# Performance work log

Hardware: AMD Instinct MI355X
Metric: run time of the kernel (lower is better)

Reference implementation:

```python
import jax, jax.numpy as jnp
import numpy as np

B, T, C, H = 2, 2048, 1024, 16


def setup_inputs() -> dict:
    key = jax.random.key(0)
    ks = jax.random.split(key, 9)
    s = 1.0 / np.sqrt(C)
    return {
        "query": jax.random.normal(ks[0], (B, T, C), dtype=jnp.float32),
        "Wq": jax.random.normal(ks[1], (C, C), dtype=jnp.float32) * s,
        "bq": jnp.zeros((C,), dtype=jnp.float32),
        "Wk": jax.random.normal(ks[2], (C, C), dtype=jnp.float32) * s,
        "bk": jnp.zeros((C,), dtype=jnp.float32),
        "Wv": jax.random.normal(ks[3], (C, C), dtype=jnp.float32) * s,
        "bv": jnp.zeros((C,), dtype=jnp.float32),
        "Wp": jax.random.normal(ks[4], (C, C), dtype=jnp.float32) * s,
        "bp": jnp.zeros((C,), dtype=jnp.float32),
        "n_head": H,
    }


def reference(query, Wq, bq, Wk, bk, Wv, bv, Wp, bp, n_head):
    b, t, c = query.shape
    d = c // n_head
    # QKV projections -> [b, h, t, d]
    q = (query @ Wq + bq).reshape(b, t, n_head, d).transpose(0, 2, 1, 3)
    k = (query @ Wk + bk).reshape(b, t, n_head, d).transpose(0, 2, 1, 3)
    v = (query @ Wv + bv).reshape(b, t, n_head, d).transpose(0, 2, 1, 3)
    scale = 1.0 / jnp.sqrt(jnp.asarray(d, dtype=query.dtype))
    att = jnp.einsum('bhtd,bhsd->bhts', q, k) * scale  # [b,h,t,t]
    causal = jnp.tril(jnp.ones((t, t), dtype=bool))
    att = jnp.where(causal[None, None, :, :], att, -jnp.inf)
    att = jax.nn.softmax(att, axis=-1)
    y = jnp.einsum('bhts,bhsd->bhtd', att, v)  # [b,h,t,d]
    y = y.transpose(0, 2, 1, 3).reshape(b, t, c)
    return y @ Wp + bp
```

## Files before the change

kernel.cpp:

```cpp
#include <hip/hip_runtime.h>
#include <math.h>

#define B_ 2
#define T_ 2048
#define C_ 1024
#define H_ 16
#define D_ 64
#define M_ (B_*T_)

typedef __bf16 bf16x8 __attribute__((ext_vector_type(8)));
typedef float  f32x4  __attribute__((ext_vector_type(4)));

__device__ __forceinline__ unsigned short f2bf(float f) {
    unsigned int u = __float_as_uint(f);
    u += 0x7FFFu + ((u >> 16) & 1u);
    return (unsigned short)(u >> 16);
}

__device__ __forceinline__ void gload16(const void* g, void* l) {
    __builtin_amdgcn_global_load_lds(
        (const __attribute__((address_space(1))) void*)g,
        (__attribute__((address_space(3))) void*)l, 16, 0, 0);
}

__global__ __launch_bounds__(256) void prep_kernel(
    const float* __restrict__ X, unsigned short* __restrict__ Xb,
    const float* __restrict__ W0, const float* __restrict__ W1,
    const float* __restrict__ W2, const float* __restrict__ W3,
    unsigned short* __restrict__ T0, unsigned short* __restrict__ T1,
    unsigned short* __restrict__ T2, unsigned short* __restrict__ T3)
{
    const int tid = threadIdx.x;
    if (blockIdx.x < 2048) {
        const size_t i = ((size_t)blockIdx.x * 256 + tid) * 8;
        const float4 a = *(const float4*)&X[i];
        const float4 b = *(const float4*)&X[i + 4];
        ushort4 s0, s1;
        s0.x = f2bf(a.x); s0.y = f2bf(a.y); s0.z = f2bf(a.z); s0.w = f2bf(a.w);
        s1.x = f2bf(b.x); s1.y = f2bf(b.y); s1.z = f2bf(b.z); s1.w = f2bf(b.w);
        *(ushort4*)&Xb[i]     = s0;
        *(ushort4*)&Xb[i + 4] = s1;
        return;
    }
    const int bz = blockIdx.x - 2048;
    const int z = bz >> 10, rem = bz & 1023;
    const float* W; unsigned short* Wt;
    switch (z) {
        case 0: W = W0; Wt = T0; break;
        case 1: W = W1; Wt = T1; break;
        case 2: W = W2; Wt = T2; break;
        default: W = W3; Wt = T3; break;
    }
    __shared__ unsigned short tile[32][33];
    const int k0 = (rem >> 5) * 32, n0 = (rem & 31) * 32;
    {
        const int r = tid >> 3, c = (tid & 7) * 4;
        const float4 v = *(const float4*)&W[(size_t)(k0 + r)*C_ + n0 + c];
        tile[c+0][r] = f2bf(v.x);
        tile[c+1][r] = f2bf(v.y);
        tile[c+2][r] = f2bf(v.z);
        tile[c+3][r] = f2bf(v.w);
    }
    __syncthreads();
    {
        const int r = tid >> 3, c = (tid & 7) * 4;
        ushort4 s;
        s.x = tile[r][c+0]; s.y = tile[r][c+1]; s.z = tile[r][c+2]; s.w = tile[r][c+3];
        *(ushort4*)&Wt[(size_t)(n0 + r)*C_ + k0 + c] = s;
    }
}

__global__ __launch_bounds__(256) void gemm_mfma_kernel(
    const unsigned short* __restrict__ A, const unsigned short* __restrict__ Bt,
    const float* __restrict__ b0, const float* __restrict__ b1,
    const float* __restrict__ b2,
    void* __restrict__ out0, void* __restrict__ out1, void* __restrict__ out2,
    int mode)
{
    __shared__ __align__(16) unsigned short Als[2][128 * 32];
    __shared__ __align__(16) unsigned short Bls[2][128 * 32];

    const int tid  = threadIdx.x;
    const int lane = tid & 63;
    const int wave = tid >> 6;
    const int wm = wave >> 1, wn = wave & 1;
    const int l15 = lane & 15, quad = lane >> 4;
    const int m0 = blockIdx.y * 128, n0 = blockIdx.x * 128;
    const int srow = lane >> 2;
    const int scol = (lane & 3) * 8;

    const f32x4 zero4 = {0.f, 0.f, 0.f, 0.f};
    f32x4 acc[4][4];
    #pragma unroll
    for (int i = 0; i < 4; ++i)
        #pragma unroll
        for (int j = 0; j < 4; ++j) acc[i][j] = zero4;

    for (int k0 = 0; k0 < C_; k0 += 64) {
        __syncthreads();
        #pragma unroll
        for (int h = 0; h < 2; ++h) {
            #pragma unroll
            for (int u = 0; u < 2; ++u) {
                const int r = wave*32 + u*16 + srow;
                gload16(&A [(size_t)(m0 + r)*C_ + k0 + h*32 + scol],
                        &Als[h][(wave*32 + u*16)*32]);
                gload16(&Bt[(size_t)(n0 + r)*C_ + k0 + h*32 + scol],
                        &Bls[h][(wave*32 + u*16)*32]);
            }
        }
        __syncthreads();

        #pragma unroll
        for (int h = 0; h < 2; ++h) {
            bf16x8 af[4], bfr[4];
            #pragma unroll
            for (int i = 0; i < 4; ++i)
                af[i] = *(const bf16x8*)&Als[h][(wm*64 + i*16 + l15)*32 + quad*8];
            #pragma unroll
            for (int j = 0; j < 4; ++j)
                bfr[j] = *(const bf16x8*)&Bls[h][(wn*64 + j*16 + l15)*32 + quad*8];

            #pragma unroll
            for (int i = 0; i < 4; ++i)
                #pragma unroll
                for (int j = 0; j < 4; ++j)
                    acc[i][j] = __builtin_amdgcn_mfma_f32_16x16x32_bf16(
                        af[i], bfr[j], acc[i][j], 0, 0, 0);
        }
    }

    if (mode == 0) {
        float* o0 = (float*)out0;
        #pragma unroll
        for (int j = 0; j < 4; ++j) {
            const int n = n0 + wn*64 + j*16 + l15;
            const float bias = b0[n];
            #pragma unroll
            for (int i = 0; i < 4; ++i)
                #pragma unroll
                for (int r = 0; r < 4; ++r) {
                    const int m = m0 + wm*64 + i*16 + quad*4 + r;
                    o0[(size_t)m*C_ + n] = acc[i][j][r] + bias;
                }
        }
        return;
    }

    __syncthreads();
    unsigned short* Ep = (wave < 2) ? &Als[wave][0] : &Bls[wave - 2][0];

    const int which = n0 >> 10;
    const int c0 = n0 & (C_ - 1);
    const int h  = (c0 >> 6) + wn;
    const int bb = m0 >> 11;
    const int t0 = (m0 & (T_ - 1)) + wm*64;
    const int bh = bb*H_ + h;
    const float* bp = (which == 0) ? b0 : (which == 1 ? b1 : b2);
    const float qscale = (which == 0) ? 0.125f : 1.0f;

    if (which < 2) {
        #pragma unroll
        for (int j = 0; j < 4; ++j) {
            const int cl = j*16 + l15;
            const float bias = bp[c0 + wn*64 + cl];
            #pragma unroll
            for (int i = 0; i < 4; ++i)
                #pragma unroll
                for (int r = 0; r < 4; ++r)
                    Ep[(i*16 + quad*4 + r)*64 + cl] =
                        f2bf((acc[i][j][r] + bias) * qscale);
        }
        unsigned short* op = (which == 0) ? (unsigned short*)out0
                                          : (unsigned short*)out1;
        const int chunk = lane & 7;
        #pragma unroll
        for (int u = 0; u < 8; ++u) {
            const int row = u*8 + (lane >> 3);
            const uint4 v = *(const uint4*)&Ep[row*64 + chunk*8];
            *(uint4*)&op[((size_t)bh*T_ + t0 + row)*D_ + chunk*8] = v;
        }
    } else {
        #pragma unroll
        for (int j = 0; j < 4; ++j) {
            const int cl = j*16 + l15;
            const float bias = bp[c0 + wn*64 + cl];
            const int xo = (l15 & 7) * 8;
            #pragma unroll
            for (int i = 0; i < 4; ++i) {
                ushort4 pk;
                pk.x = f2bf(acc[i][j][0] + bias);
                pk.y = f2bf(acc[i][j][1] + bias);
                pk.z = f2bf(acc[i][j][2] + bias);
                pk.w = f2bf(acc[i][j][3] + bias);
                *(ushort4*)&Ep[cl*64 + ((i*16 + quad*4) ^ xo)] = pk;
            }
        }
        unsigned short* op = (unsigned short*)out2;
        const int chunk = lane & 7;
        #pragma unroll
        for (int u = 0; u < 8; ++u) {
            const int d = u*8 + (lane >> 3);
            const uint4 v = *(const uint4*)&Ep[d*64 + ((chunk*8) ^ ((d & 7)*8))];
            *(uint4*)&op[((size_t)bh*D_ + d)*T_ + t0 + chunk*8] = v;
        }
    }
}

__global__ __launch_bounds__(256) void flash_mfma_kernel(
    const unsigned short* __restrict__ Qs, const unsigned short* __restrict__ Ks,
    const unsigned short* __restrict__ Vts, unsigned short* __restrict__ Y,
    float* __restrict__ part0, float* __restrict__ part1,
    float* __restrict__ lbase)
{
    static const signed char qt_tab[22] = {9,8,15,15,7,14,14,13,13,6,12,
                                           12,11,11,5,10,10,4,3,2,1,0};
    static const signed char lo_tab[22] = {0,0,0,16,0,0,15,0,14,0,0,
                                           13,0,12,0,0,11,0,0,0,0,0};
    static const signed char hi_tab[22] = {20,18,16,32,16,15,30,14,28,14,13,
                                           26,12,24,12,11,22,10,8,6,4,2};
    static const signed char pi_tab[22] = {-1,-1,10,11,-1,8,9,6,7,-1,4,
                                           5,2,3,-1,0,1,-1,-1,-1,-1,-1};

    __shared__ __align__(16) unsigned short Kls[64 * 64];
    __shared__ __align__(16) unsigned short Vls[64 * 64];
    __shared__ __align__(16) unsigned short Pls[4 * 2048];

    const int tid  = threadIdx.x;
    const int lane = tid & 63, wave = tid >> 6;
    const int l15  = lane & 15, quad = lane >> 4;
    const int job  = blockIdx.x >> 5;
    const int bh   = blockIdx.x & 31;
    const int qt   = qt_tab[job];
    const int tlo  = lo_tab[job], thi = hi_tab[job];
    const int pi   = pi_tab[job];
    const int q0   = qt * 128;
    const int qw0  = q0 + wave * 32;

    bf16x8 qf[2][2];
    #pragma unroll
    for (int i = 0; i < 2; ++i)
        #pragma unroll
        for (int kd = 0; kd < 2; ++kd)
            qf[i][kd] = *(const bf16x8*)&Qs[((size_t)bh*T_ + qw0 + i*16 + l15)*D_
                                            + kd*32 + quad*8];

    const f32x4 zero4 = {0.f, 0.f, 0.f, 0.f};
    f32x4 o[2][4];
    #pragma unroll
    for (int i = 0; i < 2; ++i)
        #pragma unroll
        for (int jd = 0; jd < 4; ++jd) o[i][jd] = zero4;
    float lsum[2] = {0.f, 0.f};

    unsigned short* Pw = &Pls[wave * 2048];
    const int kd_s = wave >> 1;
    const int c8_s = (kd_s * 4 + quad) * 8;

    for (int it = tlo; it < thi; ++it) {
        const int s0 = it * 64;
        __syncthreads();
        #pragma unroll
        for (int u = 0; u < 2; ++u) {
            const int cu  = 2*wave + u;
            const int row = ((cu & 3) << 4) + l15;
            gload16(&Ks [((size_t)bh*T_ + s0 + row)*D_ + c8_s],
                    (char*)Kls + cu*1024);
            gload16(&Vts[((size_t)bh*D_ + row)*T_ + s0 + c8_s],
                    (char*)Vls + cu*1024);
        }
        __syncthreads();

        if (s0 > qw0 + 31) continue;

        f32x4 st[2][4];
        #pragma unroll
        for (int i = 0; i < 2; ++i)
            #pragma unroll
            for (int j = 0; j < 4; ++j) st[i][j] = zero4;
        #pragma unroll
        for (int kd = 0; kd < 2; ++kd) {
            bf16x8 kf[4];
            #pragma unroll
            for (int j = 0; j < 4; ++j)
                kf[j] = *(const bf16x8*)&Kls[lane*8 + j*512 + kd*2048];
            #pragma unroll
            for (int i = 0; i < 2; ++i)
                #pragma unroll
                for (int j = 0; j < 4; ++j)
                    st[i][j] = __builtin_amdgcn_mfma_f32_16x16x32_bf16(
                        kf[j], qf[i][kd], st[i][j], 0, 0, 0);
        }

        const bool diag = (s0 + 63 > qw0);
        #pragma unroll
        for (int i = 0; i < 2; ++i) {
            const int qrow = qw0 + i*16 + l15;
            #pragma unroll
            for (int j = 0; j < 4; ++j)
                #pragma unroll
                for (int r = 0; r < 4; ++r) {
                    float e = __expf(st[i][j][r]);
                    if (diag && (s0 + j*16 + quad*4 + r > qrow)) e = 0.f;
                    st[i][j][r] = e;
                    lsum[i] += e;
                }
        }

        #pragma unroll
        for (int i = 0; i < 2; ++i)
            #pragma unroll
            for (int j = 0; j < 4; ++j) {
                ushort4 pk;
                pk.x = f2bf(st[i][j][0]); pk.y = f2bf(st[i][j][1]);
                pk.z = f2bf(st[i][j][2]); pk.w = f2bf(st[i][j][3]);
                *(ushort4*)&Pw[(((j>>1)*2 + i)*4 + (j&1)*2 + (quad>>1))*128
                               + l15*8 + (quad&1)*4] = pk;
            }

        #pragma unroll
        for (int kk = 0; kk < 2; ++kk) {
            bf16x8 pf[2], vf[4];
            #pragma unroll
            for (int i = 0; i < 2; ++i)
                pf[i] = *(const bf16x8*)&Pw[(kk*2 + i)*512 + lane*8];
            #pragma unroll
            for (int jd = 0; jd < 4; ++jd)
                vf[jd] = *(const bf16x8*)&Vls[lane*8 + jd*512 + kk*2048];
            #pragma unroll
            for (int i = 0; i < 2; ++i)
                #pragma unroll
                for (int jd = 0; jd < 4; ++jd)
                    o[i][jd] = __builtin_amdgcn_mfma_f32_16x16x32_bf16(
                        vf[jd], pf[i], o[i][jd], 0, 0, 0);
        }
    }

    #pragma unroll
    for (int i = 0; i < 2; ++i) {
        float v = lsum[i];
        v += __shfl_xor(v, 16, 64);
        v += __shfl_xor(v, 32, 64);
        lsum[i] = v;
    }

    if (pi < 0) {
        const int b = bh >> 4, h = bh & (H_ - 1);
        #pragma unroll
        for (int i = 0; i < 2; ++i) {
            const float inv = 1.0f / lsum[i];
            const int t = qw0 + i*16 + l15;
            #pragma unroll
            for (int jd = 0; jd < 4; ++jd) {
                ushort4 pk;
                pk.x = f2bf(o[i][jd][0] * inv); pk.y = f2bf(o[i][jd][1] * inv);
                pk.z = f2bf(o[i][jd][2] * inv); pk.w = f2bf(o[i][jd][3] * inv);
                *(ushort4*)&Y[((size_t)(b*T_ + t))*C_ + h*D_ + jd*16 + quad*4] = pk;
            }
        }
    } else {
        const int gpi = bh*12 + pi;
        float* Op = gpi < 256 ? part0 + (size_t)gpi*8192
                              : part1 + (size_t)(gpi-256)*8192;
        float* Lp = lbase + gpi*128;
        #pragma unroll
        for (int i = 0; i < 2; ++i) {
            const int tl = wave*32 + i*16 + l15;
            if (quad == 0) Lp[tl] = lsum[i];
            #pragma unroll
            for (int jd = 0; jd < 4; ++jd)
                *(f32x4*)&Op[(size_t)tl*64 + jd*16 + quad*4] = o[i][jd];
        }
    }
}

__global__ __launch_bounds__(256) void merge_kernel(
    const float* __restrict__ part0, const float* __restrict__ part1,
    const float* __restrict__ lbase, unsigned short* __restrict__ Y)
{
    const int pair = blockIdx.x;
    const int bh = pair / 6, qi = pair % 6;
    const int qt = 10 + qi;
    const int g0 = bh*12 + qi*2;
    const float* O0 = g0 < 256 ? part0 + (size_t)g0*8192
                               : part1 + (size_t)(g0-256)*8192;
    const float* O1 = (g0+1) < 256 ? part0 + (size_t)(g0+1)*8192
                                   : part1 + (size_t)(g0+1-256)*8192;
    const float* L0 = lbase + g0*128;
    const float* L1 = L0 + 128;

    const int tid = threadIdx.x;
    const int r = tid >> 1, c0 = (tid & 1) * 32;
    const float inv = 1.0f / (L0[r] + L1[r]);
    const int b = bh >> 4, h = bh & (H_ - 1);
    const int t = qt*128 + r;
    #pragma unroll
    for (int k = 0; k < 8; ++k) {
        const f32x4 a  = *(const f32x4*)&O0[(size_t)r*64 + c0 + k*4];
        const f32x4 bb = *(const f32x4*)&O1[(size_t)r*64 + c0 + k*4];
        ushort4 pk;
        pk.x = f2bf((a[0]+bb[0])*inv); pk.y = f2bf((a[1]+bb[1])*inv);
        pk.z = f2bf((a[2]+bb[2])*inv); pk.w = f2bf((a[3]+bb[3])*inv);
        *(ushort4*)&Y[((size_t)(b*T_ + t))*C_ + h*D_ + c0 + k*4] = pk;
    }
}

extern "C" void kernel_launch(void* const* d_in, const int* in_sizes, int n_in,
                              void* d_out, int out_size, void* d_ws, size_t ws_size,
                              hipStream_t stream) {
    const float* query = (const float*)d_in[0];
    const float* Wq = (const float*)d_in[1];
    const float* bq = (const float*)d_in[2];
    const float* Wk = (const float*)d_in[3];
    const float* bk = (const float*)d_in[4];
    const float* Wv = (const float*)d_in[5];
    const float* bv = (const float*)d_in[6];
    const float* Wp = (const float*)d_in[7];
    const float* bp = (const float*)d_in[8];
    float* out = (float*)d_out;

    char* ws = (char*)d_ws;
    unsigned short* qbf   = (unsigned short*)(ws);
    unsigned short* kbf   = (unsigned short*)(ws + 8388608);
    unsigned short* vtbf  = (unsigned short*)(ws + 16777216);
    unsigned short* WtP   = (unsigned short*)(ws + 25165824);
    unsigned short* WtQKV = (unsigned short*)(ws + 27262976);
    unsigned short* yb    = (unsigned short*)(ws + 33554432);
    unsigned short* qx    = (unsigned short*)(ws + 41943040);
    float* part0 = (float*)(ws + 41943040);
    float* part1 = (float*)(ws + 27262976);
    float* lbase = (float*)(ws + 27262976 + 4194304);

    prep_kernel<<<6144, 256, 0, stream>>>(
        query, qx, Wq, Wk, Wv, Wp,
        WtQKV, WtQKV + (size_t)C_*C_, WtQKV + 2*(size_t)C_*C_, WtP);

    gemm_mfma_kernel<<<dim3(3*C_/128, M_/128), 256, 0, stream>>>(
        qx, WtQKV, bq, bk, bv, qbf, kbf, vtbf, 1);

    flash_mfma_kernel<<<704, 256, 0, stream>>>(qbf, kbf, vtbf, yb,
                                               part0, part1, lbase);
    merge_kernel<<<192, 256, 0, stream>>>(part0, part1, lbase, yb);

    gemm_mfma_kernel<<<dim3(C_/128, M_/128), 256, 0, stream>>>(
        yb, WtP, bp, bp, bp, out, nullptr, nullptr, 0);
}
```

Measured before the change: 219.0 us.

## Rebalance causal flash attention by pairing light and heavy query tiles per block

Replaces the table-driven 22-job schedule (704 blocks) with a 16-job scheme (512 blocks). Each of the first 8 jobs processes a short query tile fully plus the first part of a long tile, and the last 8 jobs process the remainder of that long tile. This is meant to even out per-block work with fewer blocks and simpler indexing. Partial results now go into the output buffer as scratch before the final projection, and the bf16 conversions use native casts instead of manual rounding. The merge kernel now covers all 8 split tiles per head, which adds more partial-write traffic in exchange for balance.

```diff
diff --git a/kernel.cpp b/kernel.cpp
--- a/kernel.cpp
+++ b/kernel.cpp
@@ -9,6 +9,7 @@
 #define M_ (B_*T_)
 
 typedef __bf16 bf16x8 __attribute__((ext_vector_type(8)));
+typedef __bf16 bf16x4 __attribute__((ext_vector_type(4)));
 typedef float  f32x4  __attribute__((ext_vector_type(4)));
 
 __device__ __forceinline__ unsigned short f2bf(float f) {
@@ -210,18 +211,8 @@
 __global__ __launch_bounds__(256) void flash_mfma_kernel(
     const unsigned short* __restrict__ Qs, const unsigned short* __restrict__ Ks,
     const unsigned short* __restrict__ Vts, unsigned short* __restrict__ Y,
-    float* __restrict__ part0, float* __restrict__ part1,
-    float* __restrict__ lbase)
+    float* __restrict__ parts, float* __restrict__ lbase)
 {
-    static const signed char qt_tab[22] = {9,8,15,15,7,14,14,13,13,6,12,
-                                           12,11,11,5,10,10,4,3,2,1,0};
-    static const signed char lo_tab[22] = {0,0,0,16,0,0,15,0,14,0,0,
-                                           13,0,12,0,0,11,0,0,0,0,0};
-    static const signed char hi_tab[22] = {20,18,16,32,16,15,30,14,28,14,13,
-                                           26,12,24,12,11,22,10,8,6,4,2};
-    static const signed char pi_tab[22] = {-1,-1,10,11,-1,8,9,6,7,-1,4,
-                                           5,2,3,-1,0,1,-1,-1,-1,-1,-1};
-
     __shared__ __align__(16) unsigned short Kls[64 * 64];
     __shared__ __align__(16) unsigned short Vls[64 * 64];
     __shared__ __align__(16) unsigned short Pls[4 * 2048];
@@ -231,161 +222,171 @@
     const int l15  = lane & 15, quad = lane >> 4;
     const int job  = blockIdx.x >> 5;
     const int bh   = blockIdx.x & 31;
-    const int qt   = qt_tab[job];
-    const int tlo  = lo_tab[job], thi = hi_tab[job];
-    const int pi   = pi_tab[job];
-    const int q0   = qt * 128;
-    const int qw0  = q0 + wave * 32;
-
-    bf16x8 qf[2][2];
-    #pragma unroll
-    for (int i = 0; i < 2; ++i)
-        #pragma unroll
-        for (int kd = 0; kd < 2; ++kd)
-            qf[i][kd] = *(const bf16x8*)&Qs[((size_t)bh*T_ + qw0 + i*16 + l15)*D_
-                                            + kd*32 + quad*8];
-
-    const f32x4 zero4 = {0.f, 0.f, 0.f, 0.f};
-    f32x4 o[2][4];
-    #pragma unroll
-    for (int i = 0; i < 2; ++i)
-        #pragma unroll
-        for (int jd = 0; jd < 4; ++jd) o[i][jd] = zero4;
-    float lsum[2] = {0.f, 0.f};
+    const bool isA = (job < 8);
+    const int a    = isA ? job : job - 8;
+
+    int qts[2], slos[2], shis[2], slots[2], nseg;
+    if (isA) {
+        qts[0] = a;      slos[0] = 0;        shis[0] = 2*a + 2;  slots[0] = -1;
+        qts[1] = 15 - a; slos[1] = 0;        shis[1] = 15 - 2*a; slots[1] = 0;
+        nseg = 2;
+    } else {
+        qts[0] = 15 - a; slos[0] = 15 - 2*a; shis[0] = 32 - 2*a; slots[0] = 1;
+        nseg = 1;
+    }
 
     unsigned short* Pw = &Pls[wave * 2048];
     const int kd_s = wave >> 1;
     const int c8_s = (kd_s * 4 + quad) * 8;
-
-    for (int it = tlo; it < thi; ++it) {
-        const int s0 = it * 64;
-        __syncthreads();
-        #pragma unroll
-        for (int u = 0; u < 2; ++u) {
-            const int cu  = 2*wave + u;
-            const int row = ((cu & 3) << 4) + l15;
-            gload16(&Ks [((size_t)bh*T_ + s0 + row)*D_ + c8_s],
-                    (char*)Kls + cu*1024);
-            gload16(&Vts[((size_t)bh*D_ + row)*T_ + s0 + c8_s],
-                    (char*)Vls + cu*1024);
-        }
-        __syncthreads();
-
-        if (s0 > qw0 + 31) continue;
-
-        f32x4 st[2][4];
+    const int b_ = bh >> 4, h_ = bh & (H_ - 1);
+    const f32x4 zero4 = {0.f, 0.f, 0.f, 0.f};
+
+    for (int sg = 0; sg < nseg; ++sg) {
+        const int qt  = qts[sg];
+        const int qw0 = qt * 128 + wave * 32;
+
+        bf16x8 qf[2][2];
         #pragma unroll
         for (int i = 0; i < 2; ++i)
             #pragma unroll
-            for (int j = 0; j < 4; ++j) st[i][j] = zero4;
-        #pragma unroll
-        for (int kd = 0; kd < 2; ++kd) {
-            bf16x8 kf[4];
-            #pragma unroll
-            for (int j = 0; j < 4; ++j)
-                kf[j] = *(const bf16x8*)&Kls[lane*8 + j*512 + kd*2048];
+            for (int kd = 0; kd < 2; ++kd)
+                qf[i][kd] = *(const bf16x8*)&Qs[((size_t)bh*T_ + qw0 + i*16 + l15)*D_
+                                                + kd*32 + quad*8];
+
+        f32x4 o[2][4];
+        #pragma unroll
+        for (int i = 0; i < 2; ++i)
+            #pragma unroll
+            for (int jd = 0; jd < 4; ++jd) o[i][jd] = zero4;
+        float lsum[2] = {0.f, 0.f};
+
+        for (int it = slos[sg]; it < shis[sg]; ++it) {
+            const int s0 = it * 64;
+            __syncthreads();
+            #pragma unroll
+            for (int u = 0; u < 2; ++u) {
+                const int cu  = 2*wave + u;
+                const int row = ((cu & 3) << 4) + l15;
+                gload16(&Ks [((size_t)bh*T_ + s0 + row)*D_ + c8_s],
+                        (char*)Kls + cu*1024);
+                gload16(&Vts[((size_t)bh*D_ + row)*T_ + s0 + c8_s],
+                        (char*)Vls + cu*1024);
+            }
+            __syncthreads();
+
+            if (s0 > qw0 + 31) continue;
+
+            f32x4 st[2][4];
             #pragma unroll
             for (int i = 0; i < 2; ++i)
                 #pragma unroll
+                for (int j = 0; j < 4; ++j) st[i][j] = zero4;
+            #pragma unroll
+            for (int kd = 0; kd < 2; ++kd) {
+                bf16x8 kf[4];
+                #pragma unroll
                 for (int j = 0; j < 4; ++j)
-                    st[i][j] = __builtin_amdgcn_mfma_f32_16x16x32_bf16(
-                        kf[j], qf[i][kd], st[i][j], 0, 0, 0);
-        }
-
-        const bool diag = (s0 + 63 > qw0);
+                    kf[j] = *(const bf16x8*)&Kls[lane*8 + j*512 + kd*2048];
+                #pragma unroll
+                for (int i = 0; i < 2; ++i)
+                    #pragma unroll
+                    for (int j = 0; j < 4; ++j)
+                        st[i][j] = __builtin_amdgcn_mfma_f32_16x16x32_bf16(
+                            kf[j], qf[i][kd], st[i][j], 0, 0, 0);
+            }
+
+            const bool diag = (s0 + 63 > qw0);
+            #pragma unroll
+            for (int i = 0; i < 2; ++i) {
+                const int qrow = qw0 + i*16 + l15;
+                #pragma unroll
+                for (int j = 0; j < 4; ++j)
+                    #pragma unroll
+                    for (int r = 0; r < 4; ++r) {
+                        float e = __expf(st[i][j][r]);
+                        if (diag && (s0 + j*16 + quad*4 + r > qrow)) e = 0.f;
+                        st[i][j][r] = e;
+                        lsum[i] += e;
+                    }
+            }
+
+            #pragma unroll
+            for (int i = 0; i < 2; ++i)
+                #pragma unroll
+                for (int j = 0; j < 4; ++j) {
+                    bf16x4 pk = {(__bf16)st[i][j][0], (__bf16)st[i][j][1],
+                                 (__bf16)st[i][j][2], (__bf16)st[i][j][3]};
+                    *(bf16x4*)&Pw[(((j>>1)*2 + i)*4 + (j&1)*2 + (quad>>1))*128
+                                   + l15*8 + (quad&1)*4] = pk;
+                }
+
+            #pragma unroll
+            for (int kk = 0; kk < 2; ++kk) {
+                bf16x8 pf[2], vf[4];
+                #pragma unroll
+                for (int i = 0; i < 2; ++i)
+                    pf[i] = *(const bf16x8*)&Pw[(kk*2 + i)*512 + lane*8];
+                #pragma unroll
+                for (int jd = 0; jd < 4; ++jd)
+                    vf[jd] = *(const bf16x8*)&Vls[lane*8 + jd*512 + kk*2048];
+                #pragma unroll
+                for (int i = 0; i < 2; ++i)
+                    #pragma unroll
+                    for (int jd = 0; jd < 4; ++jd)
+                        o[i][jd] = __builtin_amdgcn_mfma_f32_16x16x32_bf16(
+                            vf[jd], pf[i], o[i][jd], 0, 0, 0);
+            }
+        }
+
         #pragma unroll
         for (int i = 0; i < 2; ++i) {
-            const int qrow = qw0 + i*16 + l15;
-            #pragma unroll
-            for (int j = 0; j < 4; ++j)
-                #pragma unroll
-                for (int r = 0; r < 4; ++r) {
-                    float e = __expf(st[i][j][r]);
-                    if (diag && (s0 + j*16 + quad*4 + r > qrow)) e = 0.f;
-                    st[i][j][r] = e;
-                    lsum[i] += e;
+            float v = lsum[i];
+            v += __shfl_xor(v, 16, 64);
+            v += __shfl_xor(v, 32, 64);
+            lsum[i] = v;
+        }
+
+        if (slots[sg] < 0) {
+            #pragma unroll
+            for (int i = 0; i < 2; ++i) {
+                const float inv = 1.0f / lsum[i];
+                const int t = qw0 + i*16 + l15;
+                #pragma unroll
+                for (int jd = 0; jd < 4; ++jd) {
+                    bf16x4 pk = {(__bf16)(o[i][jd][0] * inv),
+                                 (__bf16)(o[i][jd][1] * inv),
+                                 (__bf16)(o[i][jd][2] * inv),
+                                 (__bf16)(o[i][jd][3] * inv)};
+                    *(bf16x4*)&Y[((size_t)(b_*T_ + t))*C_ + h_*D_ + jd*16 + quad*4]
+                        = pk;
                 }
-        }
-
-        #pragma unroll
-        for (int i = 0; i < 2; ++i)
-            #pragma unroll
-            for (int j = 0; j < 4; ++j) {
-                ushort4 pk;
-                pk.x = f2bf(st[i][j][0]); pk.y = f2bf(st[i][j][1]);
-                pk.z = f2bf(st[i][j][2]); pk.w = f2bf(st[i][j][3]);
-                *(ushort4*)&Pw[(((j>>1)*2 + i)*4 + (j&1)*2 + (quad>>1))*128
-                               + l15*8 + (quad&1)*4] = pk;
-            }
-
-        #pragma unroll
-        for (int kk = 0; kk < 2; ++kk) {
-            bf16x8 pf[2], vf[4];
-            #pragma unroll
-            for (int i = 0; i < 2; ++i)
-                pf[i] = *(const bf16x8*)&Pw[(kk*2 + i)*512 + lane*8];
-            #pragma unroll
-            for (int jd = 0; jd < 4; ++jd)
-                vf[jd] = *(const bf16x8*)&Vls[lane*8 + jd*512 + kk*2048];
-            #pragma unroll
-            for (int i = 0; i < 2; ++i)
+            }
+        } else {
+            const int gpi = bh*16 + a*2 + slots[sg];
+            float* Op = parts + (size_t)gpi*8192;
+            float* Lp = lbase + gpi*128;
+            #pragma unroll
+            for (int i = 0; i < 2; ++i) {
+                const int tl = wave*32 + i*16 + l15;
+                if (quad == 0) Lp[tl] = lsum[i];
                 #pragma unroll
                 for (int jd = 0; jd < 4; ++jd)
-                    o[i][jd] = __builtin_amdgcn_mfma_f32_16x16x32_bf16(
-                        vf[jd], pf[i], o[i][jd], 0, 0, 0);
-        }
-    }
-
-    #pragma unroll
-    for (int i = 0; i < 2; ++i) {
-        float v = lsum[i];
-        v += __shfl_xor(v, 16, 64);
-        v += __shfl_xor(v, 32, 64);
-        lsum[i] = v;
-    }
-
-    if (pi < 0) {
-        const int b = bh >> 4, h = bh & (H_ - 1);
-        #pragma unroll
-        for (int i = 0; i < 2; ++i) {
-            const float inv = 1.0f / lsum[i];
-            const int t = qw0 + i*16 + l15;
-            #pragma unroll
-            for (int jd = 0; jd < 4; ++jd) {
-                ushort4 pk;
-                pk.x = f2bf(o[i][jd][0] * inv); pk.y = f2bf(o[i][jd][1] * inv);
-                pk.z = f2bf(o[i][jd][2] * inv); pk.w = f2bf(o[i][jd][3] * inv);
-                *(ushort4*)&Y[((size_t)(b*T_ + t))*C_ + h*D_ + jd*16 + quad*4] = pk;
-            }
-        }
-    } else {
-        const int gpi = bh*12 + pi;
-        float* Op = gpi < 256 ? part0 + (size_t)gpi*8192
-                              : part1 + (size_t)(gpi-256)*8192;
-        float* Lp = lbase + gpi*128;
-        #pragma unroll
-        for (int i = 0; i < 2; ++i) {
-            const int tl = wave*32 + i*16 + l15;
-            if (quad == 0) Lp[tl] = lsum[i];
-            #pragma unroll
-            for (int jd = 0; jd < 4; ++jd)
-                *(f32x4*)&Op[(size_t)tl*64 + jd*16 + quad*4] = o[i][jd];
+                    *(f32x4*)&Op[(size_t)tl*64 + jd*16 + quad*4] = o[i][jd];
+            }
         }
     }
 }
 
 __global__ __launch_bounds__(256) void merge_kernel(
-    const float* __restrict__ part0, const float* __restrict__ part1,
-    const float* __restrict__ lbase, unsigned short* __restrict__ Y)
+    const float* __restrict__ parts, const float* __restrict__ lbase,
+    unsigned short* __restrict__ Y)
 {
     const int pair = blockIdx.x;
-    const int bh = pair / 6, qi = pair % 6;
-    const int qt = 10 + qi;
-    const int g0 = bh*12 + qi*2;
-    const float* O0 = g0 < 256 ? part0 + (size_t)g0*8192
-                               : part1 + (size_t)(g0-256)*8192;
-    const float* O1 = (g0+1) < 256 ? part0 + (size_t)(g0+1)*8192
-                                   : part1 + (size_t)(g0+1-256)*8192;
+    const int bh = pair >> 3, p = pair & 7;
+    const int qt = 15 - p;
+    const int g0 = bh*16 + p*2;
+    const float* O0 = parts + (size_t)g0*8192;
+    const float* O1 = O0 + 8192;
     const float* L0 = lbase + g0*128;
     const float* L1 = L0 + 128;
 
@@ -398,10 +399,9 @@
     for (int k = 0; k < 8; ++k) {
         const f32x4 a  = *(const f32x4*)&O0[(size_t)r*64 + c0 + k*4];
         const f32x4 bb = *(const f32x4*)&O1[(size_t)r*64 + c0 + k*4];
-        ushort4 pk;
-        pk.x = f2bf((a[0]+bb[0])*inv); pk.y = f2bf((a[1]+bb[1])*inv);
-        pk.z = f2bf((a[2]+bb[2])*inv); pk.w = f2bf((a[3]+bb[3])*inv);
-        *(ushort4*)&Y[((size_t)(b*T_ + t))*C_ + h*D_ + c0 + k*4] = pk;
+        bf16x4 pk = {(__bf16)((a[0]+bb[0])*inv), (__bf16)((a[1]+bb[1])*inv),
+                     (__bf16)((a[2]+bb[2])*inv), (__bf16)((a[3]+bb[3])*inv)};
+        *(bf16x4*)&Y[((size_t)(b*T_ + t))*C_ + h*D_ + c0 + k*4] = pk;
     }
 }
 
@@ -427,9 +427,8 @@
     unsigned short* WtQKV = (unsigned short*)(ws + 27262976);
     unsigned short* yb    = (unsigned short*)(ws + 33554432);
     unsigned short* qx    = (unsigned short*)(ws + 41943040);
-    float* part0 = (float*)(ws + 41943040);
-    float* part1 = (float*)(ws + 27262976);
-    float* lbase = (float*)(ws + 27262976 + 4194304);
+    float* lbase = (float*)(ws + 27262976);
+    float* parts = out;
 
     prep_kernel<<<6144, 256, 0, stream>>>(
         query, qx, Wq, Wk, Wv, Wp,
@@ -438,9 +437,8 @@
     gemm_mfma_kernel<<<dim3(3*C_/128, M_/128), 256, 0, stream>>>(
         qx, WtQKV, bq, bk, bv, qbf, kbf, vtbf, 1);
 
-    flash_mfma_kernel<<<704, 256, 0, stream>>>(qbf, kbf, vtbf, yb,
-                                               part0, part1, lbase);
-    merge_kernel<<<192, 256, 0, stream>>>(part0, part1, lbase, yb);
+    flash_mfma_kernel<<<512, 256, 0, stream>>>(qbf, kbf, vtbf, yb, parts, lbase);
+    merge_kernel<<<256, 256, 0, stream>>>(parts, lbase, yb);
 
     gemm_mfma_kernel<<<dim3(C_/128, M_/128), 256, 0, stream>>>(
         yb, WtP, bp, bp, bp, out, nullptr, nullptr, 0);
```

Measured after the change: 209.4 us. 4.4% less time.
